# Optimization experiments

Measured on AMD Instinct MI355X. Metric: run time of the kernel, lower is better.

Reference implementation:

```python
import jax, jax.numpy as jnp
import numpy as np

B, S, DIN, DIM = 4, 4096, 256, 256
GAMMA = 0.9865


def setup_inputs() -> dict:
    key = jax.random.key(0)
    ks = jax.random.split(key, 9)
    inp = {
        'xq': jax.random.normal(ks[0], (B, S, DIN), dtype=jnp.float32),
        'xk': jax.random.normal(ks[1], (B, S, DIN), dtype=jnp.float32),
        'xv': jax.random.normal(ks[2], (B, S, DIN), dtype=jnp.float32),
        'Wq': jax.random.normal(ks[3], (DIN, DIM), dtype=jnp.float32) * 0.05,
        'bq': jnp.zeros((DIM,), dtype=jnp.float32),
        'Wk': jax.random.normal(ks[4], (DIN, DIM), dtype=jnp.float32) * 0.05,
        'bk': jnp.zeros((DIM,), dtype=jnp.float32),
        'Wv': jax.random.normal(ks[5], (DIN, DIM), dtype=jnp.float32) * 0.05,
        'bv': jnp.zeros((DIM,), dtype=jnp.float32),
    }
    return inp


def _decay_matrix(s, gamma):
    # D[i, j] = gamma^(i-j) if i >= j else 0
    idx = jnp.arange(s)
    diff = idx[:, None] - idx[None, :]
    D = jnp.where(diff >= 0,
                  jnp.power(jnp.float32(gamma), diff.astype(jnp.float32)),
                  jnp.float32(0.0))
    return D


def reference(xq, xk, xv, Wq, bq, Wk, bk, Wv, bv):
    Q = xq @ Wq + bq  # [B,S,D]
    K = xk @ Wk + bk  # [B,S,D]
    V = xv @ Wv + bv  # [B,S,D]
    d = Q.shape[-1]
    # scores[b,i,j] = Q[b,i] . K[b,j] / sqrt(d)
    x = jnp.einsum('bid,bjd->bij', Q, K) / jnp.sqrt(jnp.float32(d))
    D = _decay_matrix(S, GAMMA)
    # Faithful to TF broadcasting: divides along the LAST axis (per-column by
    # sqrt of that index's row-sum): D[i,j] /= sqrt(sum_k D[j,k])
    D = D / jnp.sqrt(jnp.sum(D, axis=-1))
    x = x * D  # broadcast [B,S,S] * [S,S]
    # _norm_3 per batch element with TF broadcasting: x[b,i,j] /= max(|sum_k x[b,j,k]|, 1)
    denom = jnp.maximum(jnp.abs(jnp.sum(x, axis=-1)), 1.0)  # [B,S]
    x = x / denom[:, None, :]
    return x @ V  # [B,S,D]
```

## Files before the change

kernel.cpp:

```cpp
#include <hip/hip_runtime.h>
#include <math.h>

#define BB 4
#define SS 4096
#define DD 256
#define LL 256
#define NCH 16
#define GAMMA 0.9865f
#define LOG2G (-0.019609034f)
#define INV1MG 74.07407407f
#define SLAB 1040
#define SLABB 520

typedef __attribute__((ext_vector_type(8))) short short8;
typedef __attribute__((ext_vector_type(4))) float f32x4;
typedef unsigned short u16;
typedef unsigned int u32;

__device__ __forceinline__ u16 f2bf(float f) {
  union { float f; unsigned u; } v; v.f = f;
  unsigned r = v.u + 0x7FFFu + ((v.u >> 16) & 1u);
  return (u16)(r >> 16);
}
__device__ __forceinline__ float bf2f(u16 h) {
  union { unsigned u; float f; } v; v.u = ((unsigned)h) << 16; return v.f;
}

__device__ __forceinline__ void gll16(const u16* g, u16* l) {
  __builtin_amdgcn_global_load_lds(
      (const __attribute__((address_space(1))) u32*)g,
      (__attribute__((address_space(3))) u32*)l, 16, 0, 0);
}
__device__ __forceinline__ void stage8kp(const u16* g, u16* l, int lane) {
#pragma unroll
  for (int i = 0; i < 8; ++i)
    gll16(g + i * 512 + lane * 8, l + (i >> 1) * SLAB + (i & 1) * 512);
}
__device__ __forceinline__ void stageB64(const u16* g, u16* l, int lane) {
#pragma unroll
  for (int i = 0; i < 4; ++i)
    gll16(g + i * 1024 + lane * 8, l + i * SLABB);
}

__device__ __forceinline__ void mfma_step_slab(
    const u16* Ah, const u16* Al, const u16* Bh, const u16* Bl,
    int wm0, int wn0, int fm, int fq, f32x4 acc[4][4])
{
  const int ka = fq * SLAB;
  short8 ah[4], al[4];
#pragma unroll
  for (int i = 0; i < 4; ++i) {
    ah[i] = *(const short8*)&Ah[ka + (wm0 + i * 16 + fm) * 8];
    al[i] = *(const short8*)&Al[ka + (wm0 + i * 16 + fm) * 8];
  }
#pragma unroll
  for (int j = 0; j < 4; ++j) {
    short8 bh = *(const short8*)&Bh[ka + (wn0 + j * 16 + fm) * 8];
    short8 bl = *(const short8*)&Bl[ka + (wn0 + j * 16 + fm) * 8];
#pragma unroll
    for (int i = 0; i < 4; ++i) {
      acc[i][j] = __builtin_amdgcn_mfma_f32_16x16x32_bf16(al[i], bh, acc[i][j], 0, 0, 0);
      acc[i][j] = __builtin_amdgcn_mfma_f32_16x16x32_bf16(ah[i], bl, acc[i][j], 0, 0, 0);
      acc[i][j] = __builtin_amdgcn_mfma_f32_16x16x32_bf16(ah[i], bh, acc[i][j], 0, 0, 0);
    }
  }
}

__device__ __forceinline__ void mfma_step_ab(
    const u16* Ah, const u16* Al, const u16* Bh, const u16* Bl,
    int wm0, int wn0, int fm, int fq, f32x4 acc[4][2])
{
  const int ka = fq * SLAB, kb = fq * SLABB;
  short8 ah[4], al[4];
#pragma unroll
  for (int i = 0; i < 4; ++i) {
    ah[i] = *(const short8*)&Ah[ka + (wm0 + i * 16 + fm) * 8];
    al[i] = *(const short8*)&Al[ka + (wm0 + i * 16 + fm) * 8];
  }
#pragma unroll
  for (int j = 0; j < 2; ++j) {
    short8 bh = *(const short8*)&Bh[kb + (wn0 + j * 16 + fm) * 8];
    short8 bl = *(const short8*)&Bl[kb + (wn0 + j * 16 + fm) * 8];
#pragma unroll
    for (int i = 0; i < 4; ++i) {
      acc[i][j] = __builtin_amdgcn_mfma_f32_16x16x32_bf16(al[i], bh, acc[i][j], 0, 0, 0);
      acc[i][j] = __builtin_amdgcn_mfma_f32_16x16x32_bf16(ah[i], bl, acc[i][j], 0, 0, 0);
      acc[i][j] = __builtin_amdgcn_mfma_f32_16x16x32_bf16(ah[i], bh, acc[i][j], 0, 0, 0);
    }
  }
}

__device__ __forceinline__ void bounce_write(
    float* fb, const f32x4 acc[4][4], int wm0, int wn0, int fm, int fq, int p)
{
  if (wn0 == p * 64) {
#pragma unroll
    for (int i = 0; i < 4; ++i)
#pragma unroll
      for (int j = 0; j < 4; ++j)
#pragma unroll
        for (int r = 0; r < 4; ++r)
          fb[(wm0 + i * 16 + fq * 4 + r) * 65 + j * 16 + fm] = acc[i][j][r];
  }
}

__global__ __launch_bounds__(256) void init_pack_kernel(
    const float* __restrict__ Wq, const float* __restrict__ Wk, const float* __restrict__ Wv,
    u16* __restrict__ Wth, u16* __restrict__ Wtl,
    float* __restrict__ rsP, float* __restrict__ lVec)
{
  const int which = blockIdx.x;
  const int it = blockIdx.y;
  const int t = threadIdx.x;
  if (which == 0) {
    *(float4*)&rsP[(size_t)(it * 256 + t) * 4] = (float4){0.f, 0.f, 0.f, 0.f};
  } else if (which == 1) {
    *(float4*)&lVec[(size_t)(it * 256 + t) * 4] = (float4){0.f, 0.f, 0.f, 0.f};
  }
  const float* W = which == 0 ? Wq : (which == 1 ? Wk : Wv);
  for (int pn = 0; pn < 2; ++pn) {
    int pos = it * 256 + t;
    int k8 = pos >> 7, r = pos & 127;
    u16 hs[8], ls[8];
#pragma unroll
    for (int u = 0; u < 8; ++u) {
      float x = W[(size_t)(k8 * 8 + u) * DD + pn * 128 + r];
      u16 h = f2bf(x); hs[u] = h; ls[u] = f2bf(x - bf2f(h));
    }
    size_t o = ((size_t)((which * 2 + pn) * 32 + k8)) * 1024 + (size_t)r * 8;
    *(short8*)&Wth[o] = *(short8*)hs;
    *(short8*)&Wtl[o] = *(short8*)ls;
  }
}

__global__ __launch_bounds__(256, 4) void proj_kernel(
    const float* __restrict__ xq, const float* __restrict__ xk, const float* __restrict__ xv,
    const u16* __restrict__ Wth, const u16* __restrict__ Wtl,
    const float* __restrict__ bq, const float* __restrict__ bk_, const float* __restrict__ bv,
    u16* __restrict__ Qh, u16* __restrict__ Ql,
    u16* __restrict__ Kh, u16* __restrict__ Kl,
    u16* __restrict__ KTh, u16* __restrict__ KTl, float* __restrict__ VT32,
    float* __restrict__ lVec)
{
  const int which = blockIdx.z;
  const float* bias = which == 0 ? bq : (which == 1 ? bk_ : bv);
  const int m0 = blockIdx.x * 128;
  const int pn = blockIdx.y;
  __shared__ u16 SM[4 * 4 * SLAB];
  __shared__ float rsc[128];
  __shared__ float wlut[128];
  __shared__ float kacc[64];
  float* fb = (float*)SM;
  u16* Ah = SM; u16* Al = SM + 4 * SLAB; u16* Bh = SM + 8 * SLAB; u16* Bl = SM + 12 * SLAB;
  const int tid = threadIdx.x, lane = tid & 63, wave = tid >> 6;
  const int wm0 = (wave >> 1) * 64, wn0 = (wave & 1) * 64;
  const int fm = lane & 15, fq = lane >> 4;
  if (which == 1) {
    if (tid < 128) {
      int sb = (m0 & (SS - 1)) + tid;
      rsc[tid] = rsqrtf((1.0f - exp2f((float)(sb + 1) * LOG2G)) * INV1MG);
      wlut[tid] = exp2f((float)(255 - ((m0 & (LL - 1)) + tid)) * LOG2G);
    }
    if (tid < 64) kacc[tid] = 0.f;
  }
  const float* XP = (which == 0 ? xq : (which == 1 ? xk : xv)) + (size_t)m0 * DD;
  const u16* WhP = Wth + (size_t)((which * 2 + pn) * 32) * 1024;
  const u16* WlP = Wtl + (size_t)((which * 2 + pn) * 32) * 1024;
  const int arow = tid >> 2, ak8 = tid & 3;
  f32x4 acc[4][4];
#pragma unroll
  for (int i = 0; i < 4; ++i)
#pragma unroll
    for (int j = 0; j < 4; ++j) acc[i][j] = (f32x4){0.f, 0.f, 0.f, 0.f};
  float xs[2][8];
#pragma unroll
  for (int t = 0; t < 2; ++t) {
    const float* src = XP + (size_t)(t * 64 + arow) * DD + ak8 * 8;
    *(float4*)&xs[t][0] = *(const float4*)src;
    *(float4*)&xs[t][4] = *(const float4*)(src + 4);
  }
  for (int ks = 0; ks < 8; ++ks) {
    __syncthreads();
    if (wave == 2) stage8kp(WhP + ks * 4096, Bh, lane);
    if (wave == 3) stage8kp(WlP + ks * 4096, Bl, lane);
#pragma unroll
    for (int t = 0; t < 2; ++t) {
      int row = t * 64 + arow;
      u16 hs[8], ls[8];
#pragma unroll
      for (int u = 0; u < 8; ++u) {
        u16 h = f2bf(xs[t][u]); hs[u] = h; ls[u] = f2bf(xs[t][u] - bf2f(h));
      }
      *(short8*)&Ah[ak8 * SLAB + row * 8] = *(short8*)hs;
      *(short8*)&Al[ak8 * SLAB + row * 8] = *(short8*)ls;
    }
    __syncthreads();
    if (ks < 7) {
#pragma unroll
      for (int t = 0; t < 2; ++t) {
        const float* src = XP + (size_t)(t * 64 + arow) * DD + (ks + 1) * 32 + ak8 * 8;
        *(float4*)&xs[t][0] = *(const float4*)src;
        *(float4*)&xs[t][4] = *(const float4*)(src + 4);
      }
    }
    mfma_step_slab(Ah, Al, Bh, Bl, wm0, wn0, fm, fq, acc);
  }
  const int b = m0 >> 12, sbb = m0 & (SS - 1);
  for (int p = 0; p < 2; ++p) {
    __syncthreads();
    bounce_write(fb, acc, wm0, wn0, fm, fq, p);
    __syncthreads();
    if (which == 0) {
#pragma unroll
      for (int it = 0; it < 4; ++it) {
        int unit = it * 256 + tid;
        int k8l = unit >> 7, row = unit & 127;
        int gcol0 = pn * 128 + p * 64 + k8l * 8;
        u16 hs[8], ls[8];
#pragma unroll
        for (int u = 0; u < 8; ++u) {
          float v = (fb[row * 65 + k8l * 8 + u] + bias[gcol0 + u]) * (1.f / 16.f);
          u16 h = f2bf(v); hs[u] = h; ls[u] = f2bf(v - bf2f(h));
        }
        size_t o = (size_t)(m0 >> 7) * 32768 + (size_t)(pn * 16 + p * 8 + k8l) * 1024 + row * 8;
        *(short8*)&Qh[o] = *(short8*)hs;
        *(short8*)&Ql[o] = *(short8*)ls;
      }
    } else if (which == 1) {
#pragma unroll
      for (int it = 0; it < 4; ++it) {
        int unit = it * 256 + tid;
        int k8l = unit >> 7, row = unit & 127;
        int gcol0 = pn * 128 + p * 64 + k8l * 8;
        u16 hs[8], ls[8];
#pragma unroll
        for (int u = 0; u < 8; ++u) {
          float v = (fb[row * 65 + k8l * 8 + u] + bias[gcol0 + u]) * rsc[row];
          u16 h = f2bf(v); hs[u] = h; ls[u] = f2bf(v - bf2f(h));
        }
        size_t o = (size_t)(m0 >> 7) * 32768 + (size_t)(pn * 16 + p * 8 + k8l) * 1024 + row * 8;
        *(short8*)&Kh[o] = *(short8*)hs;
        *(short8*)&Kl[o] = *(short8*)ls;
      }
      float kpart = 0.f;
#pragma unroll
      for (int it = 0; it < 4; ++it) {
        int unit = it * 256 + tid;
        int dl = unit & 63, s8l = unit >> 6;
        int gcolg = pn * 128 + p * 64 + dl;
        float bs = bias[gcolg];
        u16 hs[8], ls[8];
#pragma unroll
        for (int u = 0; u < 8; ++u) {
          int row = s8l * 8 + u;
          float v = (fb[row * 65 + dl] + bs) * rsc[row];
          kpart = fmaf(v, wlut[row], kpart);
          u16 h = f2bf(v); hs[u] = h; ls[u] = f2bf(v - bf2f(h));
        }
        int sb0 = sbb + s8l * 8;
        size_t o = ((size_t)(b * 2 + (gcolg >> 7)) * 512 + (sb0 >> 3)) * 1024 + (size_t)(gcolg & 127) * 8;
        *(short8*)&KTh[o] = *(short8*)hs;
        *(short8*)&KTl[o] = *(short8*)ls;
      }
      atomicAdd(&kacc[tid & 63], kpart);
      __syncthreads();
      if (tid < 64) {
        int c = sbb >> 8;
        atomicAdd(&lVec[(size_t)(b * NCH + c) * DD + pn * 128 + p * 64 + tid], kacc[tid]);
        kacc[tid] = 0.f;
      }
    } else {
#pragma unroll
      for (int it = 0; it < 4; ++it) {
        int unit = it * 256 + tid;
        int dl = unit & 63, s8l = unit >> 6;
        int gcolg = pn * 128 + p * 64 + dl;
        float bs = bias[gcolg];
        float vv[8];
#pragma unroll
        for (int u = 0; u < 8; ++u) vv[u] = fb[(s8l * 8 + u) * 65 + dl] + bs;
        float* dst = &VT32[(size_t)b * DD * SS + (size_t)gcolg * SS + sbb + s8l * 8];
        *(float4*)dst = (float4){vv[0], vv[1], vv[2], vv[3]};
        *(float4*)(dst + 4) = (float4){vv[4], vv[5], vv[6], vv[7]};
      }
    }
  }
}

__global__ __launch_bounds__(256, 3) void scores_kernel(
    const u16* __restrict__ Qh, const u16* __restrict__ Ql,
    const u16* __restrict__ Kh, const u16* __restrict__ Kl,
    const float* __restrict__ lVec, u16* __restrict__ Sgh, u16* __restrict__ Sgl,
    float* __restrict__ rsP)
{
  const int chunk = blockIdx.x, b = chunk >> 4, c = chunk & 15;
  const int y = blockIdx.y;
  const int m0 = (y < 2) ? 0 : 128;
  const int jn0 = (y < 2) ? y * 64 : (y - 2) * 64;
  __shared__ u16 SA[8 * SLAB];
  __shared__ u16 SB[8 * SLABB];
  __shared__ float cv[256], lut[256], rowAcc[128], qd2[2][128];
  u16* Ah = SA; u16* Al = SA + 4 * SLAB;
  u16* Bh = SB; u16* Bl = SB + 4 * SLABB;
  float* fb = (float*)SA;
  const int tid = threadIdx.x, lane = tid & 63, wave = tid >> 6;
  const int wm0 = (wave >> 1) * 64, wn0 = (wave & 1) * 32;
  const int fm = lane & 15, fq = lane >> 4;
  if (jn0 == 0) {
    const float gL = exp2f((float)LL * LOG2G);
    float s = 0.f;
    for (int cp = 0; cp < c; ++cp)
      s = fmaf(gL, s, lVec[(size_t)(b * NCH + cp) * DD + tid]);
    cv[tid] = s;
  }
  lut[tid] = exp2f((float)tid * LOG2G);
  if (tid < 128) rowAcc[tid] = 0.f;
  const int growA = b * SS + c * LL + m0;
  const int growB = b * SS + c * LL + jn0;
  const u16* QhP = Qh + (size_t)(growA >> 7) * 32768;
  const u16* QlP = Ql + (size_t)(growA >> 7) * 32768;
  const u16* KhP = Kh + (size_t)(growB >> 7) * 32768 + (size_t)(growB & 127) * 8;
  const u16* KlP = Kl + (size_t)(growB >> 7) * 32768 + (size_t)(growB & 127) * 8;
  f32x4 acc[4][2];
#pragma unroll
  for (int i = 0; i < 4; ++i)
#pragma unroll
    for (int j = 0; j < 2; ++j) acc[i][j] = (f32x4){0.f, 0.f, 0.f, 0.f};
  float qdreg = 0.f;
  const int qrow = tid & 127, qk8b = tid >> 7;
  for (int ks = 0; ks < 8; ++ks) {
    __syncthreads();
    if (wave == 0) stage8kp(QhP + ks * 4096, Ah, lane);
    if (wave == 1) stage8kp(QlP + ks * 4096, Al, lane);
    if (wave == 2) stageB64(KhP + ks * 4096, Bh, lane);
    if (wave == 3) stageB64(KlP + ks * 4096, Bl, lane);
    __syncthreads();
    mfma_step_ab(Ah, Al, Bh, Bl, wm0, wn0, fm, fq, acc);
    if (jn0 == 0) {
#pragma unroll
      for (int h2 = 0; h2 < 2; ++h2) {
        int k8l = qk8b + 2 * h2;
        const u16* ahp = &Ah[k8l * SLAB + qrow * 8];
        const u16* alp = &Al[k8l * SLAB + qrow * 8];
#pragma unroll
        for (int u = 0; u < 8; ++u)
          qdreg = fmaf(bf2f(ahp[u]) + bf2f(alp[u]), cv[ks * 32 + k8l * 8 + u], qdreg);
      }
    }
  }
  qd2[qk8b][qrow] = qdreg;
  const int ps = chunk * 2 + (m0 >> 7);
  for (int rh = 0; rh < 2; ++rh) {
    __syncthreads();
    if (wm0 == rh * 64) {
#pragma unroll
      for (int i = 0; i < 4; ++i)
#pragma unroll
        for (int j = 0; j < 2; ++j)
#pragma unroll
          for (int r = 0; r < 4; ++r)
            fb[(i * 16 + fq * 4 + r) * 65 + wn0 + j * 16 + fm] = acc[i][j][r];
    }
    __syncthreads();
#pragma unroll
    for (int it = 0; it < 2; ++it) {
      int unit = it * 256 + tid;
      int k8l = unit >> 6, rowl = unit & 63;
      int il = m0 + rh * 64 + rowl;
      int jlb = jn0 + k8l * 8;
      float part = 0.f;
      u16 hs[8], ls[8];
#pragma unroll
      for (int u = 0; u < 8; ++u) {
        int jl = jlb + u;
        float v = (jl <= il) ? fb[rowl * 65 + k8l * 8 + u] * lut[il - jl] : 0.f;
        part += v;
        u16 h = f2bf(v); hs[u] = h; ls[u] = f2bf(v - bf2f(h));
      }
      atomicAdd(&rowAcc[rh * 64 + rowl], part);
      size_t o = (size_t)(ps * 32 + (jn0 >> 3) + k8l) * 1024 + (size_t)(rh * 64 + rowl) * 8;
      *(short8*)&Sgh[o] = *(short8*)hs;
      *(short8*)&Sgl[o] = *(short8*)ls;
    }
  }
  __syncthreads();
  if (tid < 128) {
    float rs = rowAcc[tid];
    if (jn0 == 0)
      rs += exp2f((float)(m0 + tid + 1) * LOG2G) * (qd2[0][tid] + qd2[1][tid]);
    atomicAdd(&rsP[(size_t)b * SS + c * LL + m0 + tid], rs);
  }
}

__global__ __launch_bounds__(256) void vscale_kernel(
    const float* __restrict__ VT32, const float* __restrict__ rsP,
    u16* __restrict__ VdTh, u16* __restrict__ VdTl,
    u16* __restrict__ VwTh, u16* __restrict__ VwTl)
{
  const int x = blockIdx.x;
  const int b = x >> 6, pd = (x >> 5) & 1, sg = x & 31;
  const int t = threadIdx.x;
  __shared__ float tile[64][132];
  __shared__ float sdn[128], wtl[128];
  if (t < 128) {
    int s = sg * 128 + t;
    sdn[t] = fmaxf(fabsf(rsP[(size_t)b * SS + s]), 1.0f);
    wtl[t] = exp2f((float)(255 - (s & 255)) * LOG2G);
  }
  for (int eh = 0; eh < 2; ++eh) {
    __syncthreads();
#pragma unroll
    for (int v = 0; v < 8; ++v) {
      int lin = v * 256 + t;
      int col4 = lin & 31, row = lin >> 5;
      float4 xv = *(const float4*)&VT32[(size_t)b * DD * SS +
          (size_t)(pd * 128 + eh * 64 + row) * SS + sg * 128 + col4 * 4];
      *(float4*)&tile[row][col4 * 4] = xv;
    }
    __syncthreads();
#pragma unroll
    for (int it = 0; it < 4; ++it) {
      int unit = it * 256 + t;
      int s8l = unit >> 6, el = unit & 63;
      int e = pd * 128 + eh * 64 + el;
      u16 dh[8], dl_[8], wh[8], wl[8];
#pragma unroll
      for (int u = 0; u < 8; ++u) {
        int sloc = s8l * 8 + u;
        float vd = tile[el][sloc] / sdn[sloc];
        float vw = vd * wtl[sloc];
        u16 h = f2bf(vd); dh[u] = h; dl_[u] = f2bf(vd - bf2f(h));
        u16 h2 = f2bf(vw); wh[u] = h2; wl[u] = f2bf(vw - bf2f(h2));
      }
      int s8g = sg * 16 + s8l;
      size_t o = ((size_t)((b * 2 + pd) * 512 + s8g)) * 1024 + (size_t)(e & 127) * 8;
      *(short8*)&VdTh[o] = *(short8*)dh; *(short8*)&VdTl[o] = *(short8*)dl_;
      *(short8*)&VwTh[o] = *(short8*)wh; *(short8*)&VwTl[o] = *(short8*)wl;
    }
  }
}

__global__ __launch_bounds__(256, 3) void lmat_kernel(
    const u16* __restrict__ VwTh, const u16* __restrict__ VwTl,
    const u16* __restrict__ KTh, const u16* __restrict__ KTl,
    float* __restrict__ lMatT)
{
  const int chunk = blockIdx.x, b = chunk >> 4, c = chunk & 15;
  const int ty = blockIdx.y;
  const int m0 = (ty >> 2) * 128, n0 = (ty & 3) * 64;
  __shared__ u16 SA[8 * SLAB];
  __shared__ u16 SB[8 * SLABB];
  u16* Ah = SA; u16* Al = SA + 4 * SLAB;
  u16* Bh = SB; u16* Bl = SB + 4 * SLABB;
  const int tid = threadIdx.x, lane = tid & 63, wave = tid >> 6;
  const int wm0 = (wave >> 1) * 64, wn0 = (wave & 1) * 32;
  const int fm = lane & 15, fq = lane >> 4;
  const u16* AhP = VwTh + ((size_t)(b * 2 + (m0 >> 7)) * 512 + c * 32) * 1024;
  const u16* AlP = VwTl + ((size_t)(b * 2 + (m0 >> 7)) * 512 + c * 32) * 1024;
  const u16* BhP = KTh + ((size_t)(b * 2 + (n0 >> 7)) * 512 + c * 32) * 1024 + (size_t)(n0 & 127) * 8;
  const u16* BlP = KTl + ((size_t)(b * 2 + (n0 >> 7)) * 512 + c * 32) * 1024 + (size_t)(n0 & 127) * 8;
  f32x4 acc[4][2];
#pragma unroll
  for (int i = 0; i < 4; ++i)
#pragma unroll
    for (int j = 0; j < 2; ++j) acc[i][j] = (f32x4){0.f, 0.f, 0.f, 0.f};
  for (int ks = 0; ks < 8; ++ks) {
    __syncthreads();
    if (wave == 0) stage8kp(AhP + ks * 4096, Ah, lane);
    if (wave == 1) stage8kp(AlP + ks * 4096, Al, lane);
    if (wave == 2) stageB64(BhP + ks * 4096, Bh, lane);
    if (wave == 3) stageB64(BlP + ks * 4096, Bl, lane);
    __syncthreads();
    mfma_step_ab(Ah, Al, Bh, Bl, wm0, wn0, fm, fq, acc);
  }
#pragma unroll
  for (int i = 0; i < 4; ++i)
#pragma unroll
    for (int j = 0; j < 2; ++j)
#pragma unroll
      for (int r = 0; r < 4; ++r) {
        int e = m0 + wm0 + i * 16 + fq * 4 + r;
        int d = n0 + wn0 + j * 16 + fm;
        lMatT[(size_t)chunk * 65536 + (size_t)e * 256 + d] = acc[i][j][r];
      }
}

__global__ __launch_bounds__(256) void combine_mat_kernel(
    const float* __restrict__ lMatT, u16* __restrict__ cMh, u16* __restrict__ cMl)
{
  const int t = blockIdx.x * 256 + threadIdx.x;
  const int b = t >> 13, rem = t & 8191;
  const int k8 = rem >> 8, e = rem & 255;
  const float gL = powf(GAMMA, (float)LL);
  float s[8] = {0.f, 0.f, 0.f, 0.f, 0.f, 0.f, 0.f, 0.f};
  for (int ch = 0; ch < 16; ++ch) {
    size_t ro = (size_t)(b * 16 + ch) * 65536 + (size_t)e * 256 + k8 * 8;
    float4 a0 = *(const float4*)&lMatT[ro];
    float4 a1 = *(const float4*)&lMatT[ro + 4];
    float vals[8] = {a0.x, a0.y, a0.z, a0.w, a1.x, a1.y, a1.z, a1.w};
    u16 hh[8], ll[8];
#pragma unroll
    for (int u = 0; u < 8; ++u) {
      u16 h = f2bf(s[u]); hh[u] = h; ll[u] = f2bf(s[u] - bf2f(h));
    }
    size_t wo = ((size_t)(((b * 16 + ch) * 2 + (e >> 7)) * 32 + k8)) * 1024 + (size_t)(e & 127) * 8;
    *(short8*)&cMh[wo] = *(short8*)hh;
    *(short8*)&cMl[wo] = *(short8*)ll;
#pragma unroll
    for (int u = 0; u < 8; ++u) s[u] = gL * s[u] + vals[u];
  }
}

__global__ __launch_bounds__(256, 3) void out_kernel(
    const u16* __restrict__ Qh, const u16* __restrict__ Ql,
    const u16* __restrict__ cMh, const u16* __restrict__ cMl,
    const u16* __restrict__ Sgh, const u16* __restrict__ Sgl,
    const u16* __restrict__ VdTh, const u16* __restrict__ VdTl,
    float* __restrict__ out)
{
  const int chunk = blockIdx.x, b = chunk >> 4, c = chunk & 15;
  const int ty = blockIdx.y;
  const int m0 = (ty >> 2) * 128, n0 = (ty & 3) * 64;
  __shared__ u16 SA[8 * SLAB];
  __shared__ u16 SB[8 * SLABB];
  __shared__ float olut[128];
  u16* Ah = SA; u16* Al = SA + 4 * SLAB;
  u16* Bh = SB; u16* Bl = SB + 4 * SLABB;
  const int tid = threadIdx.x, lane = tid & 63, wave = tid >> 6;
  const int wm0 = (wave >> 1) * 64, wn0 = (wave & 1) * 32;
  const int fm = lane & 15, fq = lane >> 4;
  if (tid < 128) olut[tid] = exp2f((float)(m0 + tid + 1) * LOG2G);
  f32x4 acc[4][2];
#pragma unroll
  for (int i = 0; i < 4; ++i)
#pragma unroll
    for (int j = 0; j < 2; ++j) acc[i][j] = (f32x4){0.f, 0.f, 0.f, 0.f};
  {
    const u16* AhP = Qh + (size_t)(b * 32 + c * 2 + (m0 >> 7)) * 32768;
    const u16* AlP = Ql + (size_t)(b * 32 + c * 2 + (m0 >> 7)) * 32768;
    const u16* BhP = cMh + (size_t)(chunk * 2 + (n0 >> 7)) * 32768 + (size_t)(n0 & 127) * 8;
    const u16* BlP = cMl + (size_t)(chunk * 2 + (n0 >> 7)) * 32768 + (size_t)(n0 & 127) * 8;
    for (int ks = 0; ks < 8; ++ks) {
      __syncthreads();
      if (wave == 0) stage8kp(AhP + ks * 4096, Ah, lane);
      if (wave == 1) stage8kp(AlP + ks * 4096, Al, lane);
      if (wave == 2) stageB64(BhP + ks * 4096, Bh, lane);
      if (wave == 3) stageB64(BlP + ks * 4096, Bl, lane);
      __syncthreads();
      mfma_step_ab(Ah, Al, Bh, Bl, wm0, wn0, fm, fq, acc);
    }
  }
#pragma unroll
  for (int i = 0; i < 4; ++i)
#pragma unroll
    for (int r = 0; r < 4; ++r) {
      int rl = wm0 + i * 16 + fq * 4 + r;
      float sc = olut[rl];
#pragma unroll
      for (int j = 0; j < 2; ++j) acc[i][j][r] *= sc;
    }
  {
    const u16* AhP = Sgh + (size_t)(chunk * 2 + (m0 >> 7)) * 32768;
    const u16* AlP = Sgl + (size_t)(chunk * 2 + (m0 >> 7)) * 32768;
    const u16* BhP = VdTh + ((size_t)(b * 2 + (n0 >> 7)) * 512 + c * 32) * 1024 + (size_t)(n0 & 127) * 8;
    const u16* BlP = VdTl + ((size_t)(b * 2 + (n0 >> 7)) * 512 + c * 32) * 1024 + (size_t)(n0 & 127) * 8;
    const int nks = (m0 >> 5) + 4;
    for (int ks = 0; ks < nks; ++ks) {
      __syncthreads();
      if (wave == 0) stage8kp(AhP + ks * 4096, Ah, lane);
      if (wave == 1) stage8kp(AlP + ks * 4096, Al, lane);
      if (wave == 2) stageB64(BhP + ks * 4096, Bh, lane);
      if (wave == 3) stageB64(BlP + ks * 4096, Bl, lane);
      __syncthreads();
      mfma_step_ab(Ah, Al, Bh, Bl, wm0, wn0, fm, fq, acc);
    }
  }
#pragma unroll
  for (int i = 0; i < 4; ++i)
#pragma unroll
    for (int j = 0; j < 2; ++j)
#pragma unroll
      for (int r = 0; r < 4; ++r) {
        int il = m0 + wm0 + i * 16 + fq * 4 + r;
        int e = n0 + wn0 + j * 16 + fm;
        out[(size_t)(b * SS + c * LL + il) * DD + e] = acc[i][j][r];
      }
}

extern "C" void kernel_launch(void* const* d_in, const int* in_sizes, int n_in,
                              void* d_out, int out_size, void* d_ws, size_t ws_size,
                              hipStream_t stream) {
  const float* xq = (const float*)d_in[0];
  const float* xk = (const float*)d_in[1];
  const float* xv = (const float*)d_in[2];
  const float* Wq = (const float*)d_in[3];
  const float* bq = (const float*)d_in[4];
  const float* Wk = (const float*)d_in[5];
  const float* bk = (const float*)d_in[6];
  const float* Wv = (const float*)d_in[7];
  const float* bv = (const float*)d_in[8];
  float* out = (float*)d_out;

  char* p = (char*)d_ws;
  const size_t H16 = (size_t)BB * SS * DD * 2;
  u16* Qh   = (u16*)(p + 0 * H16);  u16* Ql   = (u16*)(p + 1 * H16);
  u16* Kh   = (u16*)(p + 2 * H16);  u16* Kl   = (u16*)(p + 3 * H16);
  u16* KTh  = (u16*)(p + 4 * H16);  u16* KTl  = (u16*)(p + 5 * H16);
  u16* VdTh = (u16*)(p + 6 * H16);  u16* VdTl = (u16*)(p + 7 * H16);
  u16* VwTh = (u16*)(p + 8 * H16);  u16* VwTl = (u16*)(p + 9 * H16);
  u16* Sgh  = (u16*)(p + 10 * H16); u16* Sgl  = (u16*)(p + 11 * H16);
  u16* cMh  = (u16*)(p + 12 * H16); u16* cMl  = (u16*)(p + 13 * H16);
  float* lMatT = (float*)(p + 14 * H16);
  float* VT32  = (float*)(p + 16 * H16);
  u16* Wth = (u16*)(p + 18 * H16);
  u16* Wtl = (u16*)(p + 18 * H16 + 3 * DD * DD * 2);
  float* rsP  = (float*)(p + 18 * H16 + 6 * DD * DD * 2);
  float* lVec = rsP + (size_t)BB * SS;

  init_pack_kernel<<<dim3(3, 16), 256, 0, stream>>>(Wq, Wk, Wv, Wth, Wtl, rsP, lVec);
  proj_kernel<<<dim3(BB * SS / 128, 2, 3), 256, 0, stream>>>(
      xq, xk, xv, Wth, Wtl, bq, bk, bv, Qh, Ql, Kh, Kl, KTh, KTl, VT32, lVec);
  scores_kernel<<<dim3(BB * NCH, 6), 256, 0, stream>>>(
      Qh, Ql, Kh, Kl, lVec, Sgh, Sgl, rsP);
  vscale_kernel<<<256, 256, 0, stream>>>(VT32, rsP, VdTh, VdTl, VwTh, VwTl);
  lmat_kernel<<<dim3(BB * NCH, 8), 256, 0, stream>>>(VwTh, VwTl, KTh, KTl, lMatT);
  combine_mat_kernel<<<128, 256, 0, stream>>>(lMatT, cMh, cMl);
  out_kernel<<<dim3(BB * NCH, 8), 256, 0, stream>>>(
      Qh, Ql, cMh, cMl, Sgh, Sgl, VdTh, VdTl, out);
}
```

Baseline: 219.1 us.

## Double-buffer LDS staging in the projection, scores and output GEMM loops

Each GEMM k-loop in proj, scores and the two out-stage kernels now uses two LDS buffers. The next k-slice is staged asynchronously into one buffer while MFMAs read the other, which removes one __syncthreads per iteration and overlaps global loads with compute. The slab padding shrinks from 1040 to 1032 elements to change the LDS bank mapping. The doubled LDS footprint lowers possible occupancy, and the projection kernel's launch bound drops to 2 blocks per CU.

```diff
diff --git a/kernel.cpp b/kernel.cpp
--- a/kernel.cpp
+++ b/kernel.cpp
@@ -9,7 +9,7 @@
 #define GAMMA 0.9865f
 #define LOG2G (-0.019609034f)
 #define INV1MG 74.07407407f
-#define SLAB 1040
+#define SLAB 1032
 #define SLABB 520
 
 typedef __attribute__((ext_vector_type(8))) short short8;
@@ -40,6 +40,15 @@
 #pragma unroll
   for (int i = 0; i < 4; ++i)
     gll16(g + i * 1024 + lane * 8, l + i * SLABB);
+}
+__device__ __forceinline__ void stageAB(
+    const u16* AhP, const u16* AlP, const u16* BhP, const u16* BlP, int ks,
+    u16* Ab, u16* Bb, int wave, int lane)
+{
+  if (wave == 0) stage8kp(AhP + ks * 4096, Ab, lane);
+  if (wave == 1) stage8kp(AlP + ks * 4096, Ab + 4 * SLAB, lane);
+  if (wave == 2) stageB64(BhP + ks * 4096, Bb, lane);
+  if (wave == 3) stageB64(BlP + ks * 4096, Bb + 4 * SLABB, lane);
 }
 
 __device__ __forceinline__ void mfma_step_slab(
@@ -133,7 +142,31 @@
   }
 }
 
-__global__ __launch_bounds__(256, 4) void proj_kernel(
+__device__ __forceinline__ void loadX(float xs[2][8], const float* XP, int ks,
+                                      int arow, int ak8) {
+#pragma unroll
+  for (int t = 0; t < 2; ++t) {
+    const float* src = XP + (size_t)(t * 64 + arow) * DD + ks * 32 + ak8 * 8;
+    *(float4*)&xs[t][0] = *(const float4*)src;
+    *(float4*)&xs[t][4] = *(const float4*)(src + 4);
+  }
+}
+__device__ __forceinline__ void writeAsplit(u16* Ab, const float xs[2][8],
+                                            int arow, int ak8) {
+#pragma unroll
+  for (int t = 0; t < 2; ++t) {
+    int row = t * 64 + arow;
+    u16 hs[8], ls[8];
+#pragma unroll
+    for (int u = 0; u < 8; ++u) {
+      u16 h = f2bf(xs[t][u]); hs[u] = h; ls[u] = f2bf(xs[t][u] - bf2f(h));
+    }
+    *(short8*)&Ab[ak8 * SLAB + row * 8] = *(short8*)hs;
+    *(short8*)&Ab[4 * SLAB + ak8 * SLAB + row * 8] = *(short8*)ls;
+  }
+}
+
+__global__ __launch_bounds__(256, 2) void proj_kernel(
     const float* __restrict__ xq, const float* __restrict__ xk, const float* __restrict__ xv,
     const u16* __restrict__ Wth, const u16* __restrict__ Wtl,
     const float* __restrict__ bq, const float* __restrict__ bk_, const float* __restrict__ bv,
@@ -146,12 +179,11 @@
   const float* bias = which == 0 ? bq : (which == 1 ? bk_ : bv);
   const int m0 = blockIdx.x * 128;
   const int pn = blockIdx.y;
-  __shared__ u16 SM[4 * 4 * SLAB];
+  __shared__ u16 SM[2 * 16 * SLAB];
   __shared__ float rsc[128];
   __shared__ float wlut[128];
   __shared__ float kacc[64];
   float* fb = (float*)SM;
-  u16* Ah = SM; u16* Al = SM + 4 * SLAB; u16* Bh = SM + 8 * SLAB; u16* Bl = SM + 12 * SLAB;
   const int tid = threadIdx.x, lane = tid & 63, wave = tid >> 6;
   const int wm0 = (wave >> 1) * 64, wn0 = (wave & 1) * 64;
   const int fm = lane & 15, fq = lane >> 4;
@@ -173,37 +205,24 @@
 #pragma unroll
     for (int j = 0; j < 4; ++j) acc[i][j] = (f32x4){0.f, 0.f, 0.f, 0.f};
   float xs[2][8];
-#pragma unroll
-  for (int t = 0; t < 2; ++t) {
-    const float* src = XP + (size_t)(t * 64 + arow) * DD + ak8 * 8;
-    *(float4*)&xs[t][0] = *(const float4*)src;
-    *(float4*)&xs[t][4] = *(const float4*)(src + 4);
-  }
+  loadX(xs, XP, 0, arow, ak8);
+  writeAsplit(SM, xs, arow, ak8);
+  if (wave == 2) stage8kp(WhP, SM + 8 * SLAB, lane);
+  if (wave == 3) stage8kp(WlP, SM + 12 * SLAB, lane);
+  int cur = 0;
   for (int ks = 0; ks < 8; ++ks) {
     __syncthreads();
-    if (wave == 2) stage8kp(WhP + ks * 4096, Bh, lane);
-    if (wave == 3) stage8kp(WlP + ks * 4096, Bl, lane);
-#pragma unroll
-    for (int t = 0; t < 2; ++t) {
-      int row = t * 64 + arow;
-      u16 hs[8], ls[8];
-#pragma unroll
-      for (int u = 0; u < 8; ++u) {
-        u16 h = f2bf(xs[t][u]); hs[u] = h; ls[u] = f2bf(xs[t][u] - bf2f(h));
-      }
-      *(short8*)&Ah[ak8 * SLAB + row * 8] = *(short8*)hs;
-      *(short8*)&Al[ak8 * SLAB + row * 8] = *(short8*)ls;
-    }
-    __syncthreads();
+    u16* Bc = cur ? SM + 16 * SLAB : SM;
+    u16* Bn = cur ? SM : SM + 16 * SLAB;
     if (ks < 7) {
-#pragma unroll
-      for (int t = 0; t < 2; ++t) {
-        const float* src = XP + (size_t)(t * 64 + arow) * DD + (ks + 1) * 32 + ak8 * 8;
-        *(float4*)&xs[t][0] = *(const float4*)src;
-        *(float4*)&xs[t][4] = *(const float4*)(src + 4);
-      }
-    }
-    mfma_step_slab(Ah, Al, Bh, Bl, wm0, wn0, fm, fq, acc);
+      loadX(xs, XP, ks + 1, arow, ak8);
+      if (wave == 2) stage8kp(WhP + (ks + 1) * 4096, Bn + 8 * SLAB, lane);
+      if (wave == 3) stage8kp(WlP + (ks + 1) * 4096, Bn + 12 * SLAB, lane);
+    }
+    mfma_step_slab(Bc, Bc + 4 * SLAB, Bc + 8 * SLAB, Bc + 12 * SLAB,
+                   wm0, wn0, fm, fq, acc);
+    if (ks < 7) writeAsplit(Bn, xs, arow, ak8);
+    cur ^= 1;
   }
   const int b = m0 >> 12, sbb = m0 & (SS - 1);
   for (int p = 0; p < 2; ++p) {
@@ -297,11 +316,9 @@
   const int y = blockIdx.y;
   const int m0 = (y < 2) ? 0 : 128;
   const int jn0 = (y < 2) ? y * 64 : (y - 2) * 64;
-  __shared__ u16 SA[8 * SLAB];
-  __shared__ u16 SB[8 * SLABB];
+  __shared__ u16 SA[2 * 8 * SLAB];
+  __shared__ u16 SB[2 * 8 * SLABB];
   __shared__ float cv[256], lut[256], rowAcc[128], qd2[2][128];
-  u16* Ah = SA; u16* Al = SA + 4 * SLAB;
-  u16* Bh = SB; u16* Bl = SB + 4 * SLABB;
   float* fb = (float*)SA;
   const int tid = threadIdx.x, lane = tid & 63, wave = tid >> 6;
   const int wm0 = (wave >> 1) * 64, wn0 = (wave & 1) * 32;
@@ -328,25 +345,28 @@
     for (int j = 0; j < 2; ++j) acc[i][j] = (f32x4){0.f, 0.f, 0.f, 0.f};
   float qdreg = 0.f;
   const int qrow = tid & 127, qk8b = tid >> 7;
+  stageAB(QhP, QlP, KhP, KlP, 0, SA, SB, wave, lane);
+  int cur = 0;
   for (int ks = 0; ks < 8; ++ks) {
     __syncthreads();
-    if (wave == 0) stage8kp(QhP + ks * 4096, Ah, lane);
-    if (wave == 1) stage8kp(QlP + ks * 4096, Al, lane);
-    if (wave == 2) stageB64(KhP + ks * 4096, Bh, lane);
-    if (wave == 3) stageB64(KlP + ks * 4096, Bl, lane);
-    __syncthreads();
-    mfma_step_ab(Ah, Al, Bh, Bl, wm0, wn0, fm, fq, acc);
+    u16* Ac = cur ? SA + 8 * SLAB : SA;
+    u16* Bc = cur ? SB + 8 * SLABB : SB;
+    u16* An = cur ? SA : SA + 8 * SLAB;
+    u16* Bn = cur ? SB : SB + 8 * SLABB;
+    if (ks < 7) stageAB(QhP, QlP, KhP, KlP, ks + 1, An, Bn, wave, lane);
+    mfma_step_ab(Ac, Ac + 4 * SLAB, Bc, Bc + 4 * SLABB, wm0, wn0, fm, fq, acc);
     if (jn0 == 0) {
 #pragma unroll
       for (int h2 = 0; h2 < 2; ++h2) {
         int k8l = qk8b + 2 * h2;
-        const u16* ahp = &Ah[k8l * SLAB + qrow * 8];
-        const u16* alp = &Al[k8l * SLAB + qrow * 8];
+        const u16* ahp = &Ac[k8l * SLAB + qrow * 8];
+        const u16* alp = &Ac[4 * SLAB + k8l * SLAB + qrow * 8];
 #pragma unroll
         for (int u = 0; u < 8; ++u)
           qdreg = fmaf(bf2f(ahp[u]) + bf2f(alp[u]), cv[ks * 32 + k8l * 8 + u], qdreg);
       }
     }
+    cur ^= 1;
   }
   qd2[qk8b][qrow] = qdreg;
   const int ps = chunk * 2 + (m0 >> 7);
@@ -448,10 +468,8 @@
   const int chunk = blockIdx.x, b = chunk >> 4, c = chunk & 15;
   const int ty = blockIdx.y;
   const int m0 = (ty >> 2) * 128, n0 = (ty & 3) * 64;
-  __shared__ u16 SA[8 * SLAB];
-  __shared__ u16 SB[8 * SLABB];
-  u16* Ah = SA; u16* Al = SA + 4 * SLAB;
-  u16* Bh = SB; u16* Bl = SB + 4 * SLABB;
+  __shared__ u16 SA[2 * 8 * SLAB];
+  __shared__ u16 SB[2 * 8 * SLABB];
   const int tid = threadIdx.x, lane = tid & 63, wave = tid >> 6;
   const int wm0 = (wave >> 1) * 64, wn0 = (wave & 1) * 32;
   const int fm = lane & 15, fq = lane >> 4;
@@ -464,14 +482,17 @@
   for (int i = 0; i < 4; ++i)
 #pragma unroll
     for (int j = 0; j < 2; ++j) acc[i][j] = (f32x4){0.f, 0.f, 0.f, 0.f};
+  stageAB(AhP, AlP, BhP, BlP, 0, SA, SB, wave, lane);
+  int cur = 0;
   for (int ks = 0; ks < 8; ++ks) {
     __syncthreads();
-    if (wave == 0) stage8kp(AhP + ks * 4096, Ah, lane);
-    if (wave == 1) stage8kp(AlP + ks * 4096, Al, lane);
-    if (wave == 2) stageB64(BhP + ks * 4096, Bh, lane);
-    if (wave == 3) stageB64(BlP + ks * 4096, Bl, lane);
-    __syncthreads();
-    mfma_step_ab(Ah, Al, Bh, Bl, wm0, wn0, fm, fq, acc);
+    u16* Ac = cur ? SA + 8 * SLAB : SA;
+    u16* Bc = cur ? SB + 8 * SLABB : SB;
+    u16* An = cur ? SA : SA + 8 * SLAB;
+    u16* Bn = cur ? SB : SB + 8 * SLABB;
+    if (ks < 7) stageAB(AhP, AlP, BhP, BlP, ks + 1, An, Bn, wave, lane);
+    mfma_step_ab(Ac, Ac + 4 * SLAB, Bc, Bc + 4 * SLABB, wm0, wn0, fm, fq, acc);
+    cur ^= 1;
   }
 #pragma unroll
   for (int i = 0; i < 4; ++i)
@@ -521,11 +542,9 @@
   const int chunk = blockIdx.x, b = chunk >> 4, c = chunk & 15;
   const int ty = blockIdx.y;
   const int m0 = (ty >> 2) * 128, n0 = (ty & 3) * 64;
-  __shared__ u16 SA[8 * SLAB];
-  __shared__ u16 SB[8 * SLABB];
+  __shared__ u16 SA[2 * 8 * SLAB];
+  __shared__ u16 SB[2 * 8 * SLABB];
   __shared__ float olut[128];
-  u16* Ah = SA; u16* Al = SA + 4 * SLAB;
-  u16* Bh = SB; u16* Bl = SB + 4 * SLABB;
   const int tid = threadIdx.x, lane = tid & 63, wave = tid >> 6;
   const int wm0 = (wave >> 1) * 64, wn0 = (wave & 1) * 32;
   const int fm = lane & 15, fq = lane >> 4;
@@ -535,44 +554,53 @@
   for (int i = 0; i < 4; ++i)
 #pragma unroll
     for (int j = 0; j < 2; ++j) acc[i][j] = (f32x4){0.f, 0.f, 0.f, 0.f};
+  int cur = 0;
   {
     const u16* AhP = Qh + (size_t)(b * 32 + c * 2 + (m0 >> 7)) * 32768;
     const u16* AlP = Ql + (size_t)(b * 32 + c * 2 + (m0 >> 7)) * 32768;
     const u16* BhP = cMh + (size_t)(chunk * 2 + (n0 >> 7)) * 32768 + (size_t)(n0 & 127) * 8;
     const u16* BlP = cMl + (size_t)(chunk * 2 + (n0 >> 7)) * 32768 + (size_t)(n0 & 127) * 8;
+    stageAB(AhP, AlP, BhP, BlP, 0, SA, SB, wave, lane);
     for (int ks = 0; ks < 8; ++ks) {
       __syncthreads();
-      if (wave == 0) stage8kp(AhP + ks * 4096, Ah, lane);
-      if (wave == 1) stage8kp(AlP + ks * 4096, Al, lane);
-      if (wave == 2) stageB64(BhP + ks * 4096, Bh, lane);
-      if (wave == 3) stageB64(BlP + ks * 4096, Bl, lane);
-      __syncthreads();
-      mfma_step_ab(Ah, Al, Bh, Bl, wm0, wn0, fm, fq, acc);
-    }
-  }
-#pragma unroll
-  for (int i = 0; i < 4; ++i)
-#pragma unroll
-    for (int r = 0; r < 4; ++r) {
-      int rl = wm0 + i * 16 + fq * 4 + r;
-      float sc = olut[rl];
-#pragma unroll
-      for (int j = 0; j < 2; ++j) acc[i][j][r] *= sc;
-    }
+      u16* Ac = cur ? SA + 8 * SLAB : SA;
+      u16* Bc = cur ? SB + 8 * SLABB : SB;
+      u16* An = cur ? SA : SA + 8 * SLAB;
+      u16* Bn = cur ? SB : SB + 8 * SLABB;
+      if (ks < 7) stageAB(AhP, AlP, BhP, BlP, ks + 1, An, Bn, wave, lane);
+      mfma_step_ab(Ac, Ac + 4 * SLAB, Bc, Bc + 4 * SLABB, wm0, wn0, fm, fq, acc);
+      cur ^= 1;
+    }
+  }
   {
     const u16* AhP = Sgh + (size_t)(chunk * 2 + (m0 >> 7)) * 32768;
     const u16* AlP = Sgl + (size_t)(chunk * 2 + (m0 >> 7)) * 32768;
     const u16* BhP = VdTh + ((size_t)(b * 2 + (n0 >> 7)) * 512 + c * 32) * 1024 + (size_t)(n0 & 127) * 8;
     const u16* BlP = VdTl + ((size_t)(b * 2 + (n0 >> 7)) * 512 + c * 32) * 1024 + (size_t)(n0 & 127) * 8;
     const int nks = (m0 >> 5) + 4;
+    {
+      u16* Ac = cur ? SA + 8 * SLAB : SA;
+      u16* Bc = cur ? SB + 8 * SLABB : SB;
+      stageAB(AhP, AlP, BhP, BlP, 0, Ac, Bc, wave, lane);
+    }
+#pragma unroll
+    for (int i = 0; i < 4; ++i)
+#pragma unroll
+      for (int r = 0; r < 4; ++r) {
+        int rl = wm0 + i * 16 + fq * 4 + r;
+        float sc = olut[rl];
+#pragma unroll
+        for (int j = 0; j < 2; ++j) acc[i][j][r] *= sc;
+      }
     for (int ks = 0; ks < nks; ++ks) {
       __syncthreads();
-      if (wave == 0) stage8kp(AhP + ks * 4096, Ah, lane);
-      if (wave == 1) stage8kp(AlP + ks * 4096, Al, lane);
-      if (wave == 2) stageB64(BhP + ks * 4096, Bh, lane);
-      if (wave == 3) stageB64(BlP + ks * 4096, Bl, lane);
-      __syncthreads();
-      mfma_step_ab(Ah, Al, Bh, Bl, wm0, wn0, fm, fq, acc);
+      u16* Ac = cur ? SA + 8 * SLAB : SA;
+      u16* Bc = cur ? SB + 8 * SLABB : SB;
+      u16* An = cur ? SA : SA + 8 * SLAB;
+      u16* Bn = cur ? SB : SB + 8 * SLABB;
+      if (ks + 1 < nks) stageAB(AhP, AlP, BhP, BlP, ks + 1, An, Bn, wave, lane);
+      mfma_step_ab(Ac, Ac + 4 * SLAB, Bc, Bc + 4 * SLABB, wm0, wn0, fm, fq, acc);
+      cur ^= 1;
     }
   }
 #pragma unroll
```

New measurement: 211.5 us. 1.04x faster.
